# Kernel optimization log

Hardware: AMD Instinct MI355X
Metric: run time of the kernel (lower is better)

Reference implementation:

```python
import jax, jax.numpy as jnp
import numpy as np

B, N, D = 4, 4096, 1024
QK = D // 8          # qk_dim_div = 8 -> 128
E = 2 * D            # expand_factor = 2 -> 2048


def setup_inputs() -> dict:
    key = jax.random.key(0)
    k1, k2, k3 = jax.random.split(key, 3)
    x = jax.random.normal(k1, (B, N, D), dtype=jnp.float32)
    # xavier-uniform-like scale for the fused expand / project weights
    expand = jax.random.normal(k2, (D, 2 * QK + 2 * E), dtype=jnp.float32) * np.sqrt(2.0 / (D + 2 * QK + 2 * E)).astype(np.float32)
    project = jax.random.normal(k3, (E, D), dtype=jnp.float32) * np.sqrt(2.0 / (E + D)).astype(np.float32)
    position_bias_mult = jnp.float32(4.0)
    return {"x": x, "expand": expand, "project": project, "position_bias_mult": position_bias_mult}


def _layer_norm(x, eps=1e-5):
    mu = jnp.mean(x, axis=-1, keepdims=True)
    var = jnp.mean(jnp.square(x - mu), axis=-1, keepdims=True)
    return (x - mu) * jax.lax.rsqrt(var + eps)


def reference(x, expand, project, position_bias_mult):
    d = x.shape[-1]
    qk, e = d // 8, 2 * d
    n = x.shape[1]

    nx = _layer_norm(x)
    h = nx @ expand                                    # [B, N, 2*qk + 2*e]
    q = h[..., :qk]
    k = h[..., qk:2 * qk]
    linear = h[..., 2 * qk:2 * qk + e]
    pre_gelu = h[..., 2 * qk + e:]

    gated = linear * jax.nn.gelu(pre_gelu, approximate=False)  # torch F.gelu = exact erf
    local = gated[..., :e - d]                          # [B, N, e-d]
    v = gated[..., e - d:]                              # [B, N, d]

    # learned sigmoid position bias under causal mask
    pos = jnp.arange(n)
    base = (pos[None, :] - pos[:, None]).astype(x.dtype)  # j - i
    causal = pos[None, :] <= pos[:, None]
    mask = jnp.where(causal, jax.nn.sigmoid(base + position_bias_mult), -jnp.inf)

    logits = jnp.einsum('bnq,bmq->bnm', q, k) / np.sqrt(qk).astype(np.float32) + mask
    scores = jax.nn.softmax(logits, axis=-1)            # [B, N, N]
    attn = jnp.einsum('bnm,bmd->bnd', scores, v)         # [B, N, d]

    return x + jnp.concatenate([local, attn], axis=-1) @ project
```

## Files before the change

kernel.cpp:

```cpp
#include <hip/hip_runtime.h>
#include <type_traits>

typedef __bf16 bf16x8 __attribute__((ext_vector_type(8)));
typedef __bf16 bf16x4v __attribute__((ext_vector_type(4)));
typedef float f32x4 __attribute__((ext_vector_type(4)));
typedef unsigned short u16x8 __attribute__((ext_vector_type(8)));
typedef unsigned short u16x4 __attribute__((ext_vector_type(4)));

#define NSEQ 4096
#define DM 1024
#define NBATCH 4

__device__ __forceinline__ unsigned short f2bf(float f) {
  unsigned u = __float_as_uint(f);
  u += 0x7FFFu + ((u >> 16) & 1u);
  return (unsigned short)(u >> 16);
}
__device__ __forceinline__ float bf2f(unsigned short h) {
  return __uint_as_float(((unsigned)h) << 16);
}
__device__ __forceinline__ float gelu_exact(float x) {
  return 0.5f * x * (1.0f + erff(x * 0.7071067811865475f));
}

__device__ __forceinline__ void gload_lds16(const unsigned short* src,
                                            unsigned short* dst) {
  __builtin_amdgcn_global_load_lds(
      (const __attribute__((address_space(1))) unsigned int*)src,
      (__attribute__((address_space(3))) unsigned int*)dst, 16, 0, 0);
}

__global__ __launch_bounds__(256) void ln_kernel(const float* __restrict__ x,
                                                 unsigned short* __restrict__ nx) {
  const int row = blockIdx.x;
  const int tid = threadIdx.x;
  const float4 v = reinterpret_cast<const float4*>(x + (size_t)row * DM)[tid];
  float s = v.x + v.y + v.z + v.w;
  float q = v.x * v.x + v.y * v.y + v.z * v.z + v.w * v.w;
#pragma unroll
  for (int off = 32; off > 0; off >>= 1) {
    s += __shfl_down(s, off);
    q += __shfl_down(q, off);
  }
  __shared__ float ss[4], sq[4];
  if ((tid & 63) == 0) {
    ss[tid >> 6] = s;
    sq[tid >> 6] = q;
  }
  __syncthreads();
  const float ts = ss[0] + ss[1] + ss[2] + ss[3];
  const float tq = sq[0] + sq[1] + sq[2] + sq[3];
  const float mu = ts * (1.0f / DM);
  const float var = tq * (1.0f / DM) - mu * mu;
  const float rs = rsqrtf(var + 1e-5f);
  u16x4 o;
  o[0] = f2bf((v.x - mu) * rs);
  o[1] = f2bf((v.y - mu) * rs);
  o[2] = f2bf((v.z - mu) * rs);
  o[3] = f2bf((v.w - mu) * rs);
  *reinterpret_cast<u16x4*>(nx + (size_t)row * DM + tid * 4) = o;
}

__global__ __launch_bounds__(256) void tconv_kernel(const float* __restrict__ in,
                                                    unsigned short* __restrict__ out,
                                                    int K, int N) {
  __shared__ unsigned short tile[64][72];
  const int n0 = blockIdx.x * 64;
  const int k0 = blockIdx.y * 64;
  const int tid = threadIdx.x;
  const int lr = tid >> 4, lc = (tid & 15) * 4;
#pragma unroll
  for (int p = 0; p < 4; p++) {
    const int r = lr + p * 16;
    float4 v = *reinterpret_cast<const float4*>(in + (size_t)(k0 + r) * N + n0 + lc);
    tile[r][lc + 0] = f2bf(v.x);
    tile[r][lc + 1] = f2bf(v.y);
    tile[r][lc + 2] = f2bf(v.z);
    tile[r][lc + 3] = f2bf(v.w);
  }
  __syncthreads();
  const int nn = tid >> 2, kkg = (tid & 3) * 16;
  u16x8 o0, o1;
#pragma unroll
  for (int j = 0; j < 8; j++) {
    o0[j] = tile[kkg + j][nn];
    o1[j] = tile[kkg + 8 + j][nn];
  }
  unsigned short* dst = out + (size_t)(n0 + nn) * K + k0 + kkg;
  *reinterpret_cast<u16x8*>(dst) = o0;
  *reinterpret_cast<u16x8*>(dst + 8) = o1;
}

template <bool FINAL>
__global__ __launch_bounds__(256, 4) void gemm_kernel(
    const unsigned short* __restrict__ A, int lda,
    const unsigned short* __restrict__ Bt, int ldb, void* __restrict__ Cv,
    int ldc, int K, int ntn, const float* __restrict__ X) {
  __shared__ unsigned short As[128][64];
  __shared__ unsigned short Bs[128][64];
  const int tid = threadIdx.x;
  const int bid = blockIdx.x;
  const int m0 = (bid / ntn) * 128;
  const int n0 = (bid % ntn) * 128;
  const int lane = tid & 63;
  const int w = tid >> 6;
  const int lr = lane & 15;
  const int lg = lane >> 4;
  const int wr = (w >> 1) * 64;
  const int wc = (w & 1) * 64;

  f32x4 acc[4][4];
#pragma unroll
  for (int i = 0; i < 4; i++)
#pragma unroll
    for (int j = 0; j < 4; j++)
#pragma unroll
      for (int r = 0; r < 4; r++) acc[i][j][r] = 0.0f;

  for (int k0 = 0; k0 < K; k0 += 64) {
#pragma unroll
    for (int j = 0; j < 4; j++) {
      const int boff = w * 4096 + j * 1024 + lane * 16;
      const int row = boff >> 7;
      const int col = (boff & 127) >> 1;
      gload_lds16(A + (size_t)(m0 + row) * lda + k0 + col,
                  &As[0][0] + (boff - lane * 16) / 2);
    }
#pragma unroll
    for (int j = 0; j < 4; j++) {
      const int boff = w * 4096 + j * 1024 + lane * 16;
      const int row = boff >> 7;
      const int col = (boff & 127) >> 1;
      gload_lds16(Bt + (size_t)(n0 + row) * ldb + k0 + col,
                  &Bs[0][0] + (boff - lane * 16) / 2);
    }
    __syncthreads();
#pragma unroll
    for (int kk = 0; kk < 64; kk += 32) {
      bf16x8 af[4], bfr[4];
#pragma unroll
      for (int i = 0; i < 4; i++)
        af[i] =
            *reinterpret_cast<const bf16x8*>(&As[wr + i * 16 + lr][kk + lg * 8]);
#pragma unroll
      for (int j = 0; j < 4; j++)
        bfr[j] =
            *reinterpret_cast<const bf16x8*>(&Bs[wc + j * 16 + lr][kk + lg * 8]);
#pragma unroll
      for (int i = 0; i < 4; i++)
#pragma unroll
        for (int j = 0; j < 4; j++)
          acc[i][j] = __builtin_amdgcn_mfma_f32_16x16x32_bf16(af[i], bfr[j],
                                                              acc[i][j], 0, 0, 0);
    }
    __syncthreads();
  }

  if (FINAL) {
    float* C = reinterpret_cast<float*>(Cv);
#pragma unroll
    for (int i = 0; i < 4; i++)
#pragma unroll
      for (int j = 0; j < 4; j++)
#pragma unroll
        for (int r = 0; r < 4; r++) {
          const int row = m0 + wr + i * 16 + lg * 4 + r;
          const int col = n0 + wc + j * 16 + lr;
          const size_t off = (size_t)row * ldc + col;
          C[off] = X[off] + acc[i][j][r];
        }
  } else {
    unsigned short* C = reinterpret_cast<unsigned short*>(Cv);
#pragma unroll
    for (int i = 0; i < 4; i++)
#pragma unroll
      for (int j = 0; j < 4; j++)
#pragma unroll
        for (int r = 0; r < 4; r++) {
          const int row = m0 + wr + i * 16 + lg * 4 + r;
          const int col = n0 + wc + j * 16 + lr;
          C[(size_t)row * ldc + col] = f2bf(acc[i][j][r]);
        }
  }
}

__global__ __launch_bounds__(256) void gate_local_kernel(
    const unsigned short* __restrict__ gateH, unsigned short* __restrict__ concat) {
  const int idx = blockIdx.x * 256 + threadIdx.x;
  const int row = idx >> 7;
  const int cg = idx & 127;
  const unsigned short* hr = gateH + (size_t)row * 4096;
  u16x8 lin = *reinterpret_cast<const u16x8*>(hr + cg * 8);
  u16x8 pg = *reinterpret_cast<const u16x8*>(hr + 2048 + cg * 8);
  u16x8 o;
#pragma unroll
  for (int j = 0; j < 8; j++) {
    const float l = bf2f(lin[j]);
    const float g = gelu_exact(bf2f(pg[j]));
    o[j] = f2bf(l * g);
  }
  *reinterpret_cast<u16x8*>(concat + (size_t)row * 2048 + cg * 8) = o;
}

__global__ __launch_bounds__(256) void gate_vt_kernel(
    const unsigned short* __restrict__ gateH, unsigned short* __restrict__ vT) {
  __shared__ unsigned short tbuf[64][72];
  const int n0 = blockIdx.x * 64;
  const int d0 = blockIdx.y * 64;
  const int b = blockIdx.z;
  const int tid = threadIdx.x;
#pragma unroll
  for (int p = 0; p < 2; p++) {
    const int r = p * 32 + (tid >> 3);
    const int cg = tid & 7;
    const unsigned short* hr = gateH + (size_t)(b * NSEQ + n0 + r) * 4096;
    u16x8 lin = *reinterpret_cast<const u16x8*>(hr + 1024 + d0 + cg * 8);
    u16x8 pg = *reinterpret_cast<const u16x8*>(hr + 3072 + d0 + cg * 8);
    u16x8 o;
#pragma unroll
    for (int j = 0; j < 8; j++) {
      const float l = bf2f(lin[j]);
      const float g = gelu_exact(bf2f(pg[j]));
      o[j] = f2bf(l * g);
    }
    *reinterpret_cast<u16x8*>(&tbuf[r][cg * 8]) = o;
  }
  __syncthreads();
#pragma unroll
  for (int p = 0; p < 2; p++) {
    const int d = p * 32 + (tid >> 3);
    const int ng = tid & 7;
    u16x8 o;
#pragma unroll
    for (int j = 0; j < 8; j++) o[j] = tbuf[ng * 8 + j][d];
    *reinterpret_cast<u16x8*>(vT + (size_t)(b * DM + d0 + d) * NSEQ + n0 +
                              ng * 8) = o;
  }
}

#define P_TILE 16384
#define P_PER_B 8650752
__global__ __launch_bounds__(512, 4) void pk_kernel(
    const unsigned short* __restrict__ qk, const float* __restrict__ pbm_ptr,
    unsigned short* __restrict__ P, float* __restrict__ l) {
  __shared__ unsigned short Ks[128][136];
  const int tid = threadIdx.x;
  const int lane = tid & 63;
  const int w = tid >> 6;
  const int lq = lane & 15;
  const int lg = lane >> 4;
  const int bid = blockIdx.x;
  const int b = bid / 528;
  const int t = bid - b * 528;
  int qt = (int)((sqrtf((float)(8 * t + 1)) - 1.0f) * 0.5f);
  while ((qt + 1) * (qt + 2) / 2 <= t) ++qt;
  while (qt * (qt + 1) / 2 > t) --qt;
  const int kt = t - qt * (qt + 1) / 2;
  const float pbm = *pbm_ptr;
  const float SCALE = 0.08838834764831845f;

  const unsigned short* qb = qk + (size_t)b * NSEQ * 256;

#pragma unroll
  for (int p = 0; p < 4; p++) {
    const int task = tid + p * 512;
    const int row = task >> 4;
    const int ch = task & 15;
    bf16x8 v = *reinterpret_cast<const bf16x8*>(
        qb + (size_t)(kt * 128 + row) * 256 + 128 + ch * 8);
    *reinterpret_cast<bf16x8*>(&Ks[row][ch * 8]) = v;
  }
  const int qloc = w * 16 + lq;
  bf16x8 qf[4];
#pragma unroll
  for (int ks = 0; ks < 4; ks++)
    qf[ks] = *reinterpret_cast<const bf16x8*>(
        qb + (size_t)(qt * 128 + qloc) * 256 + ks * 32 + lg * 8);
  __syncthreads();

  f32x4 sa[8];
#pragma unroll
  for (int sub = 0; sub < 8; sub++)
#pragma unroll
    for (int r = 0; r < 4; r++) sa[sub][r] = 0.0f;
#pragma unroll
  for (int ks = 0; ks < 4; ks++)
#pragma unroll
    for (int sub = 0; sub < 8; sub++) {
      bf16x8 kf =
          *reinterpret_cast<const bf16x8*>(&Ks[sub * 16 + lq][ks * 32 + lg * 8]);
      sa[sub] = __builtin_amdgcn_mfma_f32_16x16x32_bf16(kf, qf[ks], sa[sub], 0, 0, 0);
    }
  const size_t KL = (size_t)(qt + 1) * 128;
  unsigned short* Prow = P + (size_t)b * P_PER_B +
                         (size_t)(qt * (qt + 1) / 2) * P_TILE + (size_t)qloc * KL +
                         kt * 128;
  float ps = 0.0f;
  const bool diag = (kt == qt);
#pragma unroll
  for (int sub = 0; sub < 8; sub++) {
    bf16x4v pv;
#pragma unroll
    for (int r = 0; r < 4; r++) {
      const int kvloc = sub * 16 + lg * 4 + r;
      float p;
      if (diag && kvloc > qloc) {
        p = 0.0f;
      } else {
        const float dn = (float)((kt - qt) * 128 + kvloc - qloc) + pbm;
        const float s = sa[sub][r] * SCALE + 1.0f / (1.0f + __expf(-dn));
        p = __expf(s);
      }
      ps += p;
      pv[r] = (__bf16)p;
    }
    *reinterpret_cast<bf16x4v*>(Prow + sub * 16 + lg * 4) = pv;
  }
  ps += __shfl_xor(ps, 16);
  ps += __shfl_xor(ps, 32);
  if (lane < 16) atomicAdd(&l[b * NSEQ + qt * 128 + w * 16 + lane], ps);
}

__global__ __launch_bounds__(256, 4) void pv_kernel(
    const unsigned short* __restrict__ P, const unsigned short* __restrict__ vT,
    const float* __restrict__ l, unsigned short* __restrict__ concat) {
  __shared__ unsigned short As[128][64];
  __shared__ unsigned short Bs[128][64];
  const int tid = threadIdx.x;
  const int bid = blockIdx.x;
  const int qt = 31 - (bid >> 5);
  const int rest = bid & 31;
  const int b = rest >> 3;
  const int nt = rest & 7;
  const int KL = (qt + 1) * 128;
  const unsigned short* A =
      P + (size_t)b * P_PER_B + (size_t)(qt * (qt + 1) / 2) * P_TILE;
  const unsigned short* Bt = vT + (size_t)b * DM * NSEQ;
  const int n0 = nt * 128;
  const int lane = tid & 63;
  const int w = tid >> 6;
  const int lr = lane & 15;
  const int lg = lane >> 4;
  const int wr = (w >> 1) * 64;
  const int wc = (w & 1) * 64;

  f32x4 acc[4][4];
#pragma unroll
  for (int i = 0; i < 4; i++)
#pragma unroll
    for (int j = 0; j < 4; j++)
#pragma unroll
      for (int r = 0; r < 4; r++) acc[i][j][r] = 0.0f;

  for (int k0 = 0; k0 < KL; k0 += 64) {
#pragma unroll
    for (int j = 0; j < 4; j++) {
      const int boff = w * 4096 + j * 1024 + lane * 16;
      const int row = boff >> 7;
      const int col = (boff & 127) >> 1;
      gload_lds16(A + (size_t)row * KL + k0 + col,
                  &As[0][0] + (boff - lane * 16) / 2);
    }
#pragma unroll
    for (int j = 0; j < 4; j++) {
      const int boff = w * 4096 + j * 1024 + lane * 16;
      const int row = boff >> 7;
      const int col = (boff & 127) >> 1;
      gload_lds16(Bt + (size_t)(n0 + row) * NSEQ + k0 + col,
                  &Bs[0][0] + (boff - lane * 16) / 2);
    }
    __syncthreads();
#pragma unroll
    for (int kk = 0; kk < 64; kk += 32) {
      bf16x8 af[4], bfr[4];
#pragma unroll
      for (int i = 0; i < 4; i++)
        af[i] =
            *reinterpret_cast<const bf16x8*>(&As[wr + i * 16 + lr][kk + lg * 8]);
#pragma unroll
      for (int j = 0; j < 4; j++)
        bfr[j] =
            *reinterpret_cast<const bf16x8*>(&Bs[wc + j * 16 + lr][kk + lg * 8]);
#pragma unroll
      for (int i = 0; i < 4; i++)
#pragma unroll
        for (int j = 0; j < 4; j++)
          acc[i][j] = __builtin_amdgcn_mfma_f32_16x16x32_bf16(af[i], bfr[j],
                                                              acc[i][j], 0, 0, 0);
    }
    __syncthreads();
  }

  const float* lb = l + b * NSEQ + qt * 128;
#pragma unroll
  for (int i = 0; i < 4; i++) {
    f32x4 lv = *reinterpret_cast<const f32x4*>(&lb[wr + i * 16 + lg * 4]);
    f32x4 inv;
#pragma unroll
    for (int r = 0; r < 4; r++) inv[r] = 1.0f / lv[r];
#pragma unroll
    for (int j = 0; j < 4; j++)
#pragma unroll
      for (int r = 0; r < 4; r++) {
        const int grow = b * NSEQ + qt * 128 + wr + i * 16 + lg * 4 + r;
        const int col = 1024 + n0 + wc + j * 16 + lr;
        concat[(size_t)grow * 2048 + col] = f2bf(acc[i][j][r] * inv[r]);
      }
  }
}

extern "C" void kernel_launch(void* const* d_in, const int* in_sizes, int n_in,
                              void* d_out, int out_size, void* d_ws,
                              size_t ws_size, hipStream_t stream) {
  (void)in_sizes;
  (void)n_in;
  (void)out_size;
  const float* x = (const float*)d_in[0];
  const float* expand = (const float*)d_in[1];
  const float* project = (const float*)d_in[2];
  const float* pbm = (const float*)d_in[3];
  float* out = (float*)d_out;

  const size_t QK_BYTES = (size_t)16384 * 256 * 2;
  const size_t GH_BYTES = (size_t)16384 * 4096 * 2;
  const size_t CAT_BYTES = (size_t)16384 * 2048 * 2;
  const size_t NX_BYTES = (size_t)16384 * DM * 2;
  const size_t P_BYTES = (size_t)NBATCH * P_PER_B * 2;
  if (ws_size < QK_BYTES + GH_BYTES + CAT_BYTES + NX_BYTES) return;

  char* ws = (char*)d_ws;
  unsigned short* qk = (unsigned short*)ws;
  unsigned short* gateH = (unsigned short*)(ws + QK_BYTES);
  unsigned short* concat = (unsigned short*)(ws + QK_BYTES + GH_BYTES);
  unsigned short* nx = (unsigned short*)(ws + QK_BYTES + GH_BYTES + CAT_BYTES);
  unsigned short* vT = nx;
  unsigned short* projectT = nx;
  unsigned short* expandT = concat;
  unsigned short* P = gateH;
  float* l = (float*)(ws + QK_BYTES + P_BYTES);

  tconv_kernel<<<dim3(68, 16), 256, 0, stream>>>(expand, expandT, 1024, 4352);
  ln_kernel<<<16384, 256, 0, stream>>>(x, nx);
  gemm_kernel<false><<<dim3(128 * 2), 256, 0, stream>>>(
      nx, DM, expandT, DM, (void*)qk, 256, DM, 2, nullptr);
  gemm_kernel<false><<<dim3(128 * 32), 256, 0, stream>>>(
      nx, DM, expandT + (size_t)256 * DM, DM, (void*)gateH, 4096, DM, 32, nullptr);
  gate_local_kernel<<<8192, 256, 0, stream>>>(gateH, concat);
  gate_vt_kernel<<<dim3(64, 16, 4), 256, 0, stream>>>(gateH, vT);
  hipMemsetAsync(l, 0, (size_t)NBATCH * NSEQ * 4, stream);
  pk_kernel<<<dim3(NBATCH * 528), 512, 0, stream>>>(qk, pbm, P, l);
  pv_kernel<<<dim3(1024), 256, 0, stream>>>(P, vT, l, concat);
  tconv_kernel<<<dim3(16, 32), 256, 0, stream>>>(project, projectT, 2048, DM);
  gemm_kernel<true><<<dim3(128 * 8), 256, 0, stream>>>(
      concat, 2048, projectT, 2048, (void*)out, DM, 2048, 8, x);
}
```

Baseline: 494.9 us.

## Replace 128x128 GEMM with 256x256 double-buffered ping-pong pipelined GEMM

Replaces the 128x128-tile, 4-wave GEMM with a 256x256-tile, 8-wave kernel. Each K-step is split into 32-wide halves held in double-buffered LDS, and global-to-LDS prefetch is interleaved with MFMA phases using explicit s_barrier, vmcnt waits and s_setprio. The larger tiles raise arithmetic intensity and cut global traffic, while the software pipeline is meant to hide load latency behind MFMA work. In exchange it needs more registers and LDS, and launches fewer blocks (only 64 for the qk GEMM), which risks low occupancy and poor load balance.

```diff
diff --git a/kernel.cpp b/kernel.cpp
--- a/kernel.cpp
+++ b/kernel.cpp
@@ -29,6 +29,9 @@
       (const __attribute__((address_space(1))) unsigned int*)src,
       (__attribute__((address_space(3))) unsigned int*)dst, 16, 0, 0);
 }
+
+#define BAR() asm volatile("s_barrier" ::: "memory")
+#define VMCNT8() asm volatile("s_waitcnt vmcnt(8)" ::: "memory")
 
 __global__ __launch_bounds__(256) void ln_kernel(const float* __restrict__ x,
                                                  unsigned short* __restrict__ nx) {
@@ -92,94 +95,174 @@
 }
 
 template <bool FINAL>
-__global__ __launch_bounds__(256, 4) void gemm_kernel(
+__global__ __launch_bounds__(512, 2) void gemm256_kernel(
     const unsigned short* __restrict__ A, int lda,
     const unsigned short* __restrict__ Bt, int ldb, void* __restrict__ Cv,
     int ldc, int K, int ntn, const float* __restrict__ X) {
-  __shared__ unsigned short As[128][64];
-  __shared__ unsigned short Bs[128][64];
+  __shared__ unsigned short Ah[2][2][8192];
+  __shared__ unsigned short Bh[2][2][8192];
   const int tid = threadIdx.x;
-  const int bid = blockIdx.x;
-  const int m0 = (bid / ntn) * 128;
-  const int n0 = (bid % ntn) * 128;
   const int lane = tid & 63;
   const int w = tid >> 6;
-  const int lr = lane & 15;
+  const int lq = lane & 15;
   const int lg = lane >> 4;
-  const int wr = (w >> 1) * 64;
-  const int wc = (w & 1) * 64;
-
-  f32x4 acc[4][4];
-#pragma unroll
-  for (int i = 0; i < 4; i++)
+  const int wm = w >> 2;
+  const int wn = w & 3;
+  const int bid = blockIdx.x;
+  const int m0 = (bid / ntn) * 256;
+  const int n0 = (bid % ntn) * 256;
+  const int nk = K >> 6;
+
+  const int g0 = w * 64 + lane;
+  const int rowS = g0 >> 2;
+  const int kcS = (g0 & 3) * 8;
+  const unsigned short* Asrc = A + (size_t)(m0 + rowS) * lda + kcS;
+  const unsigned short* Bsrc = Bt + (size_t)(n0 + rowS) * ldb + kcS;
+  const size_t ldaj = (size_t)128 * lda;
+  const size_t ldbj = (size_t)128 * ldb;
+  const int dstW = w * 64 * 8;
+
+  auto stageA = [&](int db, int kh, int kt2) {
+    if (kt2 < nk) {
+      const unsigned short* s = Asrc + (size_t)kt2 * 64 + kh * 32;
+      unsigned short* d = &Ah[db][kh][0] + dstW;
+      gload_lds16(s, d);
+      gload_lds16(s + ldaj, d + 4096);
+    }
+  };
+  auto stageB = [&](int db, int kh, int kt2) {
+    if (kt2 < nk) {
+      const unsigned short* s = Bsrc + (size_t)kt2 * 64 + kh * 32;
+      unsigned short* d = &Bh[db][kh][0] + dstW;
+      gload_lds16(s, d);
+      gload_lds16(s + ldbj, d + 4096);
+    }
+  };
+
+  f32x4 acc[8][4];
+#pragma unroll
+  for (int i = 0; i < 8; i++)
 #pragma unroll
     for (int j = 0; j < 4; j++)
 #pragma unroll
       for (int r = 0; r < 4; r++) acc[i][j][r] = 0.0f;
 
-  for (int k0 = 0; k0 < K; k0 += 64) {
-#pragma unroll
-    for (int j = 0; j < 4; j++) {
-      const int boff = w * 4096 + j * 1024 + lane * 16;
-      const int row = boff >> 7;
-      const int col = (boff & 127) >> 1;
-      gload_lds16(A + (size_t)(m0 + row) * lda + k0 + col,
-                  &As[0][0] + (boff - lane * 16) / 2);
-    }
-#pragma unroll
-    for (int j = 0; j < 4; j++) {
-      const int boff = w * 4096 + j * 1024 + lane * 16;
-      const int row = boff >> 7;
-      const int col = (boff & 127) >> 1;
-      gload_lds16(Bt + (size_t)(n0 + row) * ldb + k0 + col,
-                  &Bs[0][0] + (boff - lane * 16) / 2);
-    }
-    __syncthreads();
-#pragma unroll
-    for (int kk = 0; kk < 64; kk += 32) {
-      bf16x8 af[4], bfr[4];
-#pragma unroll
-      for (int i = 0; i < 4; i++)
-        af[i] =
-            *reinterpret_cast<const bf16x8*>(&As[wr + i * 16 + lr][kk + lg * 8]);
-#pragma unroll
-      for (int j = 0; j < 4; j++)
-        bfr[j] =
-            *reinterpret_cast<const bf16x8*>(&Bs[wc + j * 16 + lr][kk + lg * 8]);
-#pragma unroll
-      for (int i = 0; i < 4; i++)
-#pragma unroll
-        for (int j = 0; j < 4; j++)
-          acc[i][j] = __builtin_amdgcn_mfma_f32_16x16x32_bf16(af[i], bfr[j],
-                                                              acc[i][j], 0, 0, 0);
-    }
-    __syncthreads();
+  stageA(0, 0, 0);
+  stageB(0, 0, 0);
+  stageA(0, 1, 0);
+  stageB(0, 1, 0);
+  stageA(1, 0, 1);
+  stageB(1, 0, 1);
+  VMCNT8();
+  BAR();
+
+  const int aBase = wm * 128;
+  const int bBase = wn * 64;
+
+#pragma unroll 1
+  for (int kt = 0; kt < nk; ++kt) {
+    const int buf = kt & 1;
+    bf16x8 af[4], bf0[4], bf1[4];
+
+#pragma unroll
+    for (int i = 0; i < 4; i++)
+      af[i] = *reinterpret_cast<const bf16x8*>(
+          &Ah[buf][0][(aBase + i * 16 + lq) * 32 + lg * 8]);
+#pragma unroll
+    for (int j = 0; j < 4; j++)
+      bf0[j] = *reinterpret_cast<const bf16x8*>(
+          &Bh[buf][0][(bBase + j * 16 + lq) * 32 + lg * 8]);
+    stageA(buf ^ 1, 1, kt + 1);
+    BAR();
+    __builtin_amdgcn_s_setprio(1);
+#pragma unroll
+    for (int i = 0; i < 4; i++)
+#pragma unroll
+      for (int j = 0; j < 4; j++)
+        acc[i][j] =
+            __builtin_amdgcn_mfma_f32_16x16x32_bf16(af[i], bf0[j], acc[i][j], 0, 0, 0);
+    __builtin_amdgcn_s_setprio(0);
+    BAR();
+
+#pragma unroll
+    for (int i = 0; i < 4; i++)
+      af[i] = *reinterpret_cast<const bf16x8*>(
+          &Ah[buf][0][(aBase + 64 + i * 16 + lq) * 32 + lg * 8]);
+    stageB(buf ^ 1, 1, kt + 1);
+    VMCNT8();
+    BAR();
+    __builtin_amdgcn_s_setprio(1);
+#pragma unroll
+    for (int i = 0; i < 4; i++)
+#pragma unroll
+      for (int j = 0; j < 4; j++)
+        acc[4 + i][j] = __builtin_amdgcn_mfma_f32_16x16x32_bf16(af[i], bf0[j],
+                                                                acc[4 + i][j], 0, 0, 0);
+    __builtin_amdgcn_s_setprio(0);
+    BAR();
+
+#pragma unroll
+    for (int i = 0; i < 4; i++)
+      af[i] = *reinterpret_cast<const bf16x8*>(
+          &Ah[buf][1][(aBase + i * 16 + lq) * 32 + lg * 8]);
+#pragma unroll
+    for (int j = 0; j < 4; j++)
+      bf1[j] = *reinterpret_cast<const bf16x8*>(
+          &Bh[buf][1][(bBase + j * 16 + lq) * 32 + lg * 8]);
+    stageA(buf, 0, kt + 2);
+    BAR();
+    __builtin_amdgcn_s_setprio(1);
+#pragma unroll
+    for (int i = 0; i < 4; i++)
+#pragma unroll
+      for (int j = 0; j < 4; j++)
+        acc[i][j] =
+            __builtin_amdgcn_mfma_f32_16x16x32_bf16(af[i], bf1[j], acc[i][j], 0, 0, 0);
+    __builtin_amdgcn_s_setprio(0);
+    BAR();
+
+#pragma unroll
+    for (int i = 0; i < 4; i++)
+      af[i] = *reinterpret_cast<const bf16x8*>(
+          &Ah[buf][1][(aBase + 64 + i * 16 + lq) * 32 + lg * 8]);
+    stageB(buf, 0, kt + 2);
+    VMCNT8();
+    BAR();
+    __builtin_amdgcn_s_setprio(1);
+#pragma unroll
+    for (int i = 0; i < 4; i++)
+#pragma unroll
+      for (int j = 0; j < 4; j++)
+        acc[4 + i][j] = __builtin_amdgcn_mfma_f32_16x16x32_bf16(af[i], bf1[j],
+                                                                acc[4 + i][j], 0, 0, 0);
+    __builtin_amdgcn_s_setprio(0);
+    BAR();
   }
 
   if (FINAL) {
     float* C = reinterpret_cast<float*>(Cv);
 #pragma unroll
-    for (int i = 0; i < 4; i++)
+    for (int I = 0; I < 8; I++)
 #pragma unroll
       for (int j = 0; j < 4; j++)
 #pragma unroll
         for (int r = 0; r < 4; r++) {
-          const int row = m0 + wr + i * 16 + lg * 4 + r;
-          const int col = n0 + wc + j * 16 + lr;
+          const int row = m0 + wm * 128 + I * 16 + lg * 4 + r;
+          const int col = n0 + wn * 64 + j * 16 + lq;
           const size_t off = (size_t)row * ldc + col;
-          C[off] = X[off] + acc[i][j][r];
+          C[off] = X[off] + acc[I][j][r];
         }
   } else {
     unsigned short* C = reinterpret_cast<unsigned short*>(Cv);
 #pragma unroll
-    for (int i = 0; i < 4; i++)
+    for (int I = 0; I < 8; I++)
 #pragma unroll
       for (int j = 0; j < 4; j++)
 #pragma unroll
         for (int r = 0; r < 4; r++) {
-          const int row = m0 + wr + i * 16 + lg * 4 + r;
-          const int col = n0 + wc + j * 16 + lr;
-          C[(size_t)row * ldc + col] = f2bf(acc[i][j][r]);
+          const int row = m0 + wm * 128 + I * 16 + lg * 4 + r;
+          const int col = n0 + wn * 64 + j * 16 + lq;
+          C[(size_t)row * ldc + col] = f2bf(acc[I][j][r]);
         }
   }
 }
@@ -441,16 +524,16 @@
 
   tconv_kernel<<<dim3(68, 16), 256, 0, stream>>>(expand, expandT, 1024, 4352);
   ln_kernel<<<16384, 256, 0, stream>>>(x, nx);
-  gemm_kernel<false><<<dim3(128 * 2), 256, 0, stream>>>(
-      nx, DM, expandT, DM, (void*)qk, 256, DM, 2, nullptr);
-  gemm_kernel<false><<<dim3(128 * 32), 256, 0, stream>>>(
-      nx, DM, expandT + (size_t)256 * DM, DM, (void*)gateH, 4096, DM, 32, nullptr);
+  gemm256_kernel<false><<<dim3(64), 512, 0, stream>>>(
+      nx, DM, expandT, DM, (void*)qk, 256, DM, 1, nullptr);
+  gemm256_kernel<false><<<dim3(64 * 16), 512, 0, stream>>>(
+      nx, DM, expandT + (size_t)256 * DM, DM, (void*)gateH, 4096, DM, 16, nullptr);
   gate_local_kernel<<<8192, 256, 0, stream>>>(gateH, concat);
   gate_vt_kernel<<<dim3(64, 16, 4), 256, 0, stream>>>(gateH, vT);
   hipMemsetAsync(l, 0, (size_t)NBATCH * NSEQ * 4, stream);
   pk_kernel<<<dim3(NBATCH * 528), 512, 0, stream>>>(qk, pbm, P, l);
   pv_kernel<<<dim3(1024), 256, 0, stream>>>(P, vT, l, concat);
   tconv_kernel<<<dim3(16, 32), 256, 0, stream>>>(project, projectT, 2048, DM);
-  gemm_kernel<true><<<dim3(128 * 8), 256, 0, stream>>>(
-      concat, 2048, projectT, 2048, (void*)out, DM, 2048, 8, x);
-}
+  gemm256_kernel<true><<<dim3(64 * 4), 512, 0, stream>>>(
+      concat, 2048, projectT, 2048, (void*)out, DM, 2048, 4, x);
+}
```

New measurement: 494.0 us. No clear change (-0.2%).
